# Kernel optimization log

Measured on AMD Instinct MI355X. Metric: run time of the kernel, lower is better.

## Reference

```python
import jax, jax.numpy as jnp
import numpy as np

N = 100000      # nodes
E = 1600000     # edges
IN = 128        # in_channels
H = 128         # hidden_channels
OUT = 40        # out_channels
EPS = 1e-5      # BatchNorm eps


def setup_inputs() -> dict:
    key = jax.random.key(0)
    ks = jax.random.split(key, 16)
    s_in = 1.0 / np.sqrt(IN)
    s_h = 1.0 / np.sqrt(H)
    s_fc = 1.0 / np.sqrt(IN + 2 * H)
    return {
        "x": jax.random.normal(ks[0], (N, IN), dtype=jnp.float32),
        "edge_index": jax.random.randint(ks[1], (2, E), 0, N, dtype=jnp.int32),
        "W1": jax.random.normal(ks[2], (IN, H), dtype=jnp.float32) * s_in,
        "b1": jnp.zeros((H,), dtype=jnp.float32),
        "W2": jax.random.normal(ks[3], (H, H), dtype=jnp.float32) * s_h,
        "b2": jnp.zeros((H,), dtype=jnp.float32),
        "bn1_gamma": jnp.ones((H,), dtype=jnp.float32),
        "bn1_beta": jnp.zeros((H,), dtype=jnp.float32),
        "bn1_mean": jax.random.normal(ks[4], (H,), dtype=jnp.float32) * 0.1,
        "bn1_var": jax.random.uniform(ks[5], (H,), dtype=jnp.float32, minval=0.5, maxval=1.5),
        "bn2_gamma": jnp.ones((H,), dtype=jnp.float32),
        "bn2_beta": jnp.zeros((H,), dtype=jnp.float32),
        "bn2_mean": jax.random.normal(ks[6], (H,), dtype=jnp.float32) * 0.1,
        "bn2_var": jax.random.uniform(ks[7], (H,), dtype=jnp.float32, minval=0.5, maxval=1.5),
        "fc_W": jax.random.normal(ks[8], (IN + 2 * H, OUT), dtype=jnp.float32) * s_fc,
        "fc_b": jnp.zeros((OUT,), dtype=jnp.float32),
    }


def _gcn_conv(x, edge_index, W, b):
    """PyG GCNConv: symmetric norm with self-loops. x:[N,F_in] -> [N,F_out]."""
    row, col = edge_index[0], edge_index[1]  # messages flow col -> row
    h = x @ W                                 # [N, F_out] transform first
    deg = jax.ops.segment_sum(jnp.ones((E,), x.dtype), row, num_segments=N) + 1.0  # +1 self-loop
    dinv = jax.lax.rsqrt(deg)                 # deg^{-1/2}
    norm = dinv[row] * dinv[col]              # [E]
    msg = h[col] * norm[:, None]              # gather + scale
    agg = jax.ops.segment_sum(msg, row, num_segments=N)
    agg = agg + h * (dinv * dinv)[:, None]    # self-loop contribution
    return agg + b


def _bn_eval(x, gamma, beta, mean, var):
    return (x - mean) * (gamma * jax.lax.rsqrt(var + EPS)) + beta


def reference(x, edge_index, W1, b1, W2, b2,
              bn1_gamma, bn1_beta, bn1_mean, bn1_var,
              bn2_gamma, bn2_beta, bn2_mean, bn2_var,
              fc_W, fc_b):
    x0 = x
    x1 = _gcn_conv(x0, edge_index, W1, b1)
    x1 = jax.nn.relu(_bn_eval(x1, bn1_gamma, bn1_beta, bn1_mean, bn1_var))
    # dropout: eval mode -> identity
    x2 = _gcn_conv(x1, edge_index, W2, b2)
    x2 = jax.nn.relu(_bn_eval(x2, bn2_gamma, bn2_beta, bn2_mean, bn2_var))
    out = jnp.concatenate([x0, x1, x2], axis=-1) @ fc_W + fc_b  # [N, OUT]
    return out
```

## Files before the change

kernel.cpp:

```cpp
#include <hip/hip_runtime.h>

#define N_NODES 100000
#define N_EDGES 1600000
#define C_H     128
#define C_OUT   40
#define K_FC    384
#define BN_EPS  1e-5f
#define NB      391
#define CHUNK   6144

typedef unsigned int uint;

__global__ void zero_i32(int* p, int n) {
    int i = blockIdx.x * blockDim.x + threadIdx.x;
    if (i < n) p[i] = 0;
}

__global__ __launch_bounds__(256) void bucket_count(const int* __restrict__ erow,
                                                    int* __restrict__ bcnt) {
    __shared__ int cnt[NB];
    for (int i = threadIdx.x; i < NB; i += 256) cnt[i] = 0;
    __syncthreads();
    const int c0 = blockIdx.x * CHUNK;
    const int c1 = min(c0 + CHUNK, N_EDGES);
    for (int e = c0 + threadIdx.x; e < c1; e += 256)
        atomicAdd(&cnt[erow[e] >> 8], 1);
    __syncthreads();
    for (int i = threadIdx.x; i < NB; i += 256)
        if (cnt[i]) atomicAdd(&bcnt[i], cnt[i]);
}

__global__ __launch_bounds__(256) void scan_buckets(const int* __restrict__ bcnt,
                                                    int* __restrict__ bstart,
                                                    int* __restrict__ bfill) {
    __shared__ int sa[512], sb[512];
    const int t = threadIdx.x;
    int v0 = (t < NB) ? bcnt[t] : 0;
    int v1 = (t + 256 < NB) ? bcnt[t + 256] : 0;
    sa[t] = v0; sa[t + 256] = v1;
    __syncthreads();
    int* src = sa; int* dst = sb;
    for (int off = 1; off < 512; off <<= 1) {
        dst[t]       = src[t]       + (t >= off ? src[t - off] : 0);
        dst[t + 256] = src[t + 256] + (t + 256 >= off ? src[t + 256 - off] : 0);
        __syncthreads();
        int* tmp = src; src = dst; dst = tmp;
    }
    if (t < NB)       { bstart[t] = src[t] - v0;             bfill[t] = src[t] - v0; }
    if (t + 256 < NB) { bstart[t + 256] = src[t + 256] - v1; bfill[t + 256] = src[t + 256] - v1; }
    if (t == 0) bstart[NB] = N_EDGES;
}

__global__ __launch_bounds__(256) void bucket_bin(const int* __restrict__ erow,
                                                  const int* __restrict__ ecol,
                                                  int* __restrict__ bfill,
                                                  int2* __restrict__ pairs) {
    __shared__ int cnt[NB];
    __shared__ int lpos[NB];
    for (int i = threadIdx.x; i < NB; i += 256) cnt[i] = 0;
    __syncthreads();
    const int c0 = blockIdx.x * CHUNK;
    const int c1 = min(c0 + CHUNK, N_EDGES);
    for (int e = c0 + threadIdx.x; e < c1; e += 256)
        atomicAdd(&cnt[erow[e] >> 8], 1);
    __syncthreads();
    for (int i = threadIdx.x; i < NB; i += 256)
        lpos[i] = cnt[i] ? atomicAdd(&bfill[i], cnt[i]) : 0;
    __syncthreads();
    for (int e = c0 + threadIdx.x; e < c1; e += 256) {
        int r = erow[e], c = ecol[e];
        int p = atomicAdd(&lpos[r >> 8], 1);
        pairs[p] = make_int2(r, c);
    }
}

__global__ __launch_bounds__(256) void bucket_csr(const int2* __restrict__ pairs,
                                                  const int* __restrict__ bstart,
                                                  int* __restrict__ rowptr,
                                                  float* __restrict__ dinv,
                                                  int* __restrict__ colsg) {
    __shared__ int lcnt[256], sa[256], sb[256], lpos[256];
    const int b = blockIdx.x;
    const int t = threadIdx.x;
    const int p0 = bstart[b], p1 = bstart[b + 1];
    lcnt[t] = 0;
    __syncthreads();
    for (int i = p0 + t; i < p1; i += 256)
        atomicAdd(&lcnt[pairs[i].x & 255], 1);
    __syncthreads();
    sa[t] = lcnt[t];
    __syncthreads();
    int* src = sa; int* dst = sb;
    for (int off = 1; off < 256; off <<= 1) {
        dst[t] = src[t] + (t >= off ? src[t - off] : 0);
        __syncthreads();
        int* tmp = src; src = dst; dst = tmp;
    }
    const int excl = src[t] - lcnt[t];
    const int r = b * 256 + t;
    if (r < N_NODES) {
        rowptr[r] = p0 + excl;
        dinv[r] = rsqrtf((float)lcnt[t] + 1.0f);
    }
    if (b == NB - 1 && t == 0) rowptr[N_NODES] = N_EDGES;
    lpos[t] = excl;
    __syncthreads();
    for (int i = p0 + t; i < p1; i += 256) {
        int2 pr = pairs[i];
        int s = atomicAdd(&lpos[pr.x & 255], 1);
        colsg[p0 + s] = pr.y;
    }
}

__global__ void bn_coef(const float* b1, const float* g1, const float* be1,
                        const float* m1, const float* v1,
                        const float* b2, const float* g2, const float* be2,
                        const float* m2, const float* v2,
                        float* s1, float* t1, float* s2, float* t2) {
    int f = threadIdx.x;
    float sa = g1[f] * rsqrtf(v1[f] + BN_EPS);
    s1[f] = sa;
    t1[f] = (b1[f] - m1[f]) * sa + be1[f];
    float sb = g2[f] * rsqrtf(v2[f] + BN_EPS);
    s2[f] = sb;
    t2[f] = (b2[f] - m2[f]) * sb + be2[f];
}

#define FMA4(A, S, V) \
    A.x = fmaf(S, V.x, A.x); A.y = fmaf(S, V.y, A.y); \
    A.z = fmaf(S, V.z, A.z); A.w = fmaf(S, V.w, A.w);

__device__ inline uint pack_bf16x2(float a, float b) {
    uint ua = __builtin_bit_cast(uint, a);
    uint ub = __builtin_bit_cast(uint, b);
    ua += 0x7fffu + ((ua >> 16) & 1u);
    ub += 0x7fffu + ((ub >> 16) & 1u);
    return (ua >> 16) | (ub & 0xffff0000u);
}

__global__ __launch_bounds__(256) void gemm_scaled(const float* __restrict__ X,
                                                   const float* __restrict__ W,
                                                   const float* __restrict__ dinv,
                                                   uint* __restrict__ Hs) {
    __shared__ float wl[64 * 128];
    __shared__ float xl[32 * 68];

    const int tid = threadIdx.x;
    const int rg = tid >> 5;
    const int c4 = (tid & 31) << 2;
    const int rb = blockIdx.x * 32;
    const int r0 = rb + rg * 4;

    float4 acc0 = {0,0,0,0}, acc1 = {0,0,0,0}, acc2 = {0,0,0,0}, acc3 = {0,0,0,0};

    for (int half = 0; half < 2; ++half) {
        const int k0 = half * 64;
        __syncthreads();
        {
            const float4* W4 = (const float4*)(W + (size_t)k0 * 128);
            float4* wl4 = (float4*)wl;
            #pragma unroll
            for (int i = 0; i < 8; ++i) wl4[tid + i * 256] = W4[tid + i * 256];
        }
        #pragma unroll
        for (int i = 0; i < 2; ++i) {
            int f = tid + i * 256;
            int row = f >> 4, cc = f & 15;
            float4 v = *(const float4*)(X + (size_t)(rb + row) * 128 + k0 + cc * 4);
            *(float4*)&xl[row * 68 + cc * 4] = v;
        }
        __syncthreads();

        for (int k4 = 0; k4 < 16; ++k4) {
            const float* wr = wl + k4 * 4 * 128 + c4;
            float4 w0 = *(const float4*)(wr);
            float4 w1 = *(const float4*)(wr + 128);
            float4 w2 = *(const float4*)(wr + 256);
            float4 w3 = *(const float4*)(wr + 384);
            float4 xv0 = *(const float4*)&xl[(rg * 4 + 0) * 68 + k4 * 4];
            float4 xv1 = *(const float4*)&xl[(rg * 4 + 1) * 68 + k4 * 4];
            float4 xv2 = *(const float4*)&xl[(rg * 4 + 2) * 68 + k4 * 4];
            float4 xv3 = *(const float4*)&xl[(rg * 4 + 3) * 68 + k4 * 4];
            FMA4(acc0, xv0.x, w0) FMA4(acc0, xv0.y, w1) FMA4(acc0, xv0.z, w2) FMA4(acc0, xv0.w, w3)
            FMA4(acc1, xv1.x, w0) FMA4(acc1, xv1.y, w1) FMA4(acc1, xv1.z, w2) FMA4(acc1, xv1.w, w3)
            FMA4(acc2, xv2.x, w0) FMA4(acc2, xv2.y, w1) FMA4(acc2, xv2.z, w2) FMA4(acc2, xv2.w, w3)
            FMA4(acc3, xv3.x, w0) FMA4(acc3, xv3.y, w1) FMA4(acc3, xv3.z, w2) FMA4(acc3, xv3.w, w3)
        }
    }
    float d0 = dinv[r0], d1 = dinv[r0 + 1], d2 = dinv[r0 + 2], d3 = dinv[r0 + 3];
    uint2 o;
    o.x = pack_bf16x2(acc0.x * d0, acc0.y * d0);
    o.y = pack_bf16x2(acc0.z * d0, acc0.w * d0);
    *(uint2*)(Hs + (size_t)(r0 + 0) * 64 + (c4 >> 1)) = o;
    o.x = pack_bf16x2(acc1.x * d1, acc1.y * d1);
    o.y = pack_bf16x2(acc1.z * d1, acc1.w * d1);
    *(uint2*)(Hs + (size_t)(r0 + 1) * 64 + (c4 >> 1)) = o;
    o.x = pack_bf16x2(acc2.x * d2, acc2.y * d2);
    o.y = pack_bf16x2(acc2.z * d2, acc2.w * d2);
    *(uint2*)(Hs + (size_t)(r0 + 2) * 64 + (c4 >> 1)) = o;
    o.x = pack_bf16x2(acc3.x * d3, acc3.y * d3);
    o.y = pack_bf16x2(acc3.z * d3, acc3.w * d3);
    *(uint2*)(Hs + (size_t)(r0 + 3) * 64 + (c4 >> 1)) = o;
}

#define ACC1(V) \
    accx += __builtin_bit_cast(float, V << 16); \
    accy += __builtin_bit_cast(float, V & 0xffff0000u);

__global__ __launch_bounds__(256) void spmm_bn_relu4(
    const uint* __restrict__ Hs, const int* __restrict__ cols,
    const int* __restrict__ rowptr, const float* __restrict__ dinv,
    const float* __restrict__ s, const float* __restrict__ t,
    float* __restrict__ Y) {
    const int lane = threadIdx.x & 63;
    const int r = blockIdx.x * 4 + (threadIdx.x >> 6);

    uint vself = Hs[(size_t)r * 64 + lane];
    float accx = __builtin_bit_cast(float, vself << 16);
    float accy = __builtin_bit_cast(float, vself & 0xffff0000u);
    const float di = dinv[r];
    const int e0 = rowptr[r], e1 = rowptr[r + 1];
    int j = e0;
    const int n16 = e0 + ((e1 - e0) & ~15);
    for (; j < n16; j += 16) {
        uint v[16];
        #pragma unroll
        for (int q = 0; q < 16; ++q)
            v[q] = Hs[(size_t)cols[j + q] * 64 + lane];
        #pragma unroll
        for (int q = 0; q < 16; ++q) { ACC1(v[q]) }
    }
    const int n4 = e0 + ((e1 - e0) & ~3);
    for (; j < n4; j += 4) {
        uint v[4];
        #pragma unroll
        for (int q = 0; q < 4; ++q)
            v[q] = Hs[(size_t)cols[j + q] * 64 + lane];
        #pragma unroll
        for (int q = 0; q < 4; ++q) { ACC1(v[q]) }
    }
    for (; j < e1; ++j) {
        uint v0 = Hs[(size_t)cols[j] * 64 + lane];
        ACC1(v0)
    }
    float2 sf = ((const float2*)s)[lane];
    float2 tf = ((const float2*)t)[lane];
    float2 o;
    o.x = fmaxf(fmaf(accx * di, sf.x, tf.x), 0.0f);
    o.y = fmaxf(fmaf(accy * di, sf.y, tf.y), 0.0f);
    ((float2*)Y)[(size_t)r * 64 + lane] = o;
}

__global__ __launch_bounds__(256) void final_gemm7(
    const float* __restrict__ X0, const float* __restrict__ X1,
    const float* __restrict__ X2, const float* __restrict__ fcW,
    const float* __restrict__ fcb, float* __restrict__ out) {
    __shared__ float xs[2][64 * 33];

    const int t = threadIdx.x;
    const int lane = t & 63;
    const int wq = __builtin_amdgcn_readfirstlane(t >> 6);
    const float* wbase = fcW + wq * 10;
    const int rbase = blockIdx.x * 64;

    float acc[10];
    #pragma unroll
    for (int c = 0; c < 10; ++c) acc[c] = 0.0f;

    const float* segs[3] = {X0, X1, X2};
    float4 xr[2];

    auto load_chunk = [&](int ch) {
        const float* xseg = segs[ch >> 2];
        const int koff = (ch & 3) * 32;
        #pragma unroll
        for (int i = 0; i < 2; ++i) {
            int f = t + i * 256;
            int row = f >> 3, cc = f & 7;
            int r = rbase + row;
            float4 v = {0, 0, 0, 0};
            if (r < N_NODES)
                v = *(const float4*)(xseg + (size_t)r * 128 + koff + cc * 4);
            xr[i] = v;
        }
    };

    auto store_chunk = [&](int buf) {
        #pragma unroll
        for (int i = 0; i < 2; ++i) {
            int f = t + i * 256;
            int row = f >> 3, cc = f & 7;
            float* p = &xs[buf][row * 33 + cc * 4];
            p[0] = xr[i].x; p[1] = xr[i].y; p[2] = xr[i].z; p[3] = xr[i].w;
        }
    };

    load_chunk(0);
    for (int ch = 0; ch < 12; ++ch) {
        const int buf = ch & 1;
        store_chunk(buf);
        if (ch < 11) load_chunk(ch + 1);
        __syncthreads();
        const int k0 = ch * 32;
        #pragma unroll
        for (int kk4 = 0; kk4 < 8; ++kk4) {
            float xv[4];
            #pragma unroll
            for (int j = 0; j < 4; ++j)
                xv[j] = xs[buf][lane * 33 + kk4 * 4 + j];
            #pragma unroll
            for (int j = 0; j < 4; ++j) {
                const float* wr = wbase + (size_t)(k0 + kk4 * 4 + j) * 40;
                #pragma unroll
                for (int c = 0; c < 10; ++c)
                    acc[c] = fmaf(xv[j], wr[c], acc[c]);
            }
        }
    }

    const int r = rbase + lane;
    if (r < N_NODES) {
        #pragma unroll
        for (int c2 = 0; c2 < 5; ++c2) {
            float2 o;
            o.x = acc[c2 * 2 + 0] + fcb[wq * 10 + c2 * 2 + 0];
            o.y = acc[c2 * 2 + 1] + fcb[wq * 10 + c2 * 2 + 1];
            *(float2*)(out + (size_t)r * 40 + wq * 10 + c2 * 2) = o;
        }
    }
}

extern "C" void kernel_launch(void* const* d_in, const int* in_sizes, int n_in,
                              void* d_out, int out_size, void* d_ws, size_t ws_size,
                              hipStream_t stream) {
    const float* x   = (const float*)d_in[0];
    const int*   ei  = (const int*)d_in[1];
    const int* e_row = ei;
    const int* e_col = ei + N_EDGES;
    const float* W1  = (const float*)d_in[2];
    const float* b1  = (const float*)d_in[3];
    const float* W2  = (const float*)d_in[4];
    const float* b2  = (const float*)d_in[5];
    const float* g1  = (const float*)d_in[6];
    const float* be1 = (const float*)d_in[7];
    const float* m1  = (const float*)d_in[8];
    const float* v1  = (const float*)d_in[9];
    const float* g2  = (const float*)d_in[10];
    const float* be2 = (const float*)d_in[11];
    const float* m2  = (const float*)d_in[12];
    const float* v2  = (const float*)d_in[13];
    const float* fcW = (const float*)d_in[14];
    const float* fcb = (const float*)d_in[15];
    float* out = (float*)d_out;

    char* ws = (char*)d_ws;
    size_t off = 0;
    auto alloc = [&](size_t b) {
        char* p = ws + off;
        off += (b + 255) & ~(size_t)255;
        return p;
    };
    uint*  h      = (uint*)alloc((size_t)N_NODES * C_H * 2);
    float* x1     = (float*)alloc((size_t)N_NODES * C_H * 4);
    float* x2     = (float*)alloc((size_t)N_NODES * C_H * 4);
    int2*  pairs  = (int2*)alloc((size_t)N_EDGES * 8);
    int*   cols   = (int*)alloc((size_t)N_EDGES * 4);
    float* dinv   = (float*)alloc(N_NODES * 4);
    int*   rowptr = (int*)alloc((N_NODES + 1) * 4);
    int*   bcnt   = (int*)alloc((NB + 1) * 4);
    int*   bstart = (int*)alloc((NB + 1) * 4);
    int*   bfill  = (int*)alloc((NB + 1) * 4);
    float* coef   = (float*)alloc(512 * 4);
    float* s1 = coef, *t1 = coef + 128, *s2 = coef + 256, *t2 = coef + 384;

    const int nwg_bin = (N_EDGES + CHUNK - 1) / CHUNK;

    zero_i32<<<2, 256, 0, stream>>>(bcnt, NB);
    bucket_count<<<nwg_bin, 256, 0, stream>>>(e_row, bcnt);
    scan_buckets<<<1, 256, 0, stream>>>(bcnt, bstart, bfill);
    bucket_bin<<<nwg_bin, 256, 0, stream>>>(e_row, e_col, bfill, pairs);
    bucket_csr<<<NB, 256, 0, stream>>>(pairs, bstart, rowptr, dinv, cols);
    bn_coef<<<1, 128, 0, stream>>>(b1, g1, be1, m1, v1, b2, g2, be2, m2, v2,
                                   s1, t1, s2, t2);

    gemm_scaled<<<N_NODES / 32, 256, 0, stream>>>(x, W1, dinv, h);
    spmm_bn_relu4<<<N_NODES / 4, 256, 0, stream>>>(h, cols, rowptr, dinv, s1, t1, x1);
    gemm_scaled<<<N_NODES / 32, 256, 0, stream>>>(x1, W2, dinv, h);
    spmm_bn_relu4<<<N_NODES / 4, 256, 0, stream>>>(h, cols, rowptr, dinv, s2, t2, x2);
    final_gemm7<<<(N_NODES + 63) / 64, 256, 0, stream>>>(x, x1, x2, fcW, fcb, out);
}
```

Baseline: 519.1 us.

## Triple-buffer final GEMM shared tiles with two-chunk-ahead register prefetch

```diff
diff --git a/kernel.cpp b/kernel.cpp
--- a/kernel.cpp
+++ b/kernel.cpp
@@ -251,11 +251,11 @@
     ((float2*)Y)[(size_t)r * 64 + lane] = o;
 }
 
-__global__ __launch_bounds__(256) void final_gemm7(
+__global__ __launch_bounds__(256) void final_gemm9(
     const float* __restrict__ X0, const float* __restrict__ X1,
     const float* __restrict__ X2, const float* __restrict__ fcW,
     const float* __restrict__ fcb, float* __restrict__ out) {
-    __shared__ float xs[2][64 * 33];
+    __shared__ float xs[3 * 64 * 33];
 
     const int t = threadIdx.x;
     const int lane = t & 63;
@@ -267,56 +267,78 @@
     #pragma unroll
     for (int c = 0; c < 10; ++c) acc[c] = 0.0f;
 
-    const float* segs[3] = {X0, X1, X2};
-    float4 xr[2];
-
-    auto load_chunk = [&](int ch) {
-        const float* xseg = segs[ch >> 2];
-        const int koff = (ch & 3) * 32;
-        #pragma unroll
-        for (int i = 0; i < 2; ++i) {
-            int f = t + i * 256;
-            int row = f >> 3, cc = f & 7;
-            int r = rbase + row;
-            float4 v = {0, 0, 0, 0};
-            if (r < N_NODES)
-                v = *(const float4*)(xseg + (size_t)r * 128 + koff + cc * 4);
-            xr[i] = v;
-        }
-    };
-
-    auto store_chunk = [&](int buf) {
-        #pragma unroll
-        for (int i = 0; i < 2; ++i) {
-            int f = t + i * 256;
-            int row = f >> 3, cc = f & 7;
-            float* p = &xs[buf][row * 33 + cc * 4];
-            p[0] = xr[i].x; p[1] = xr[i].y; p[2] = xr[i].z; p[3] = xr[i].w;
-        }
-    };
-
-    load_chunk(0);
-    for (int ch = 0; ch < 12; ++ch) {
-        const int buf = ch & 1;
-        store_chunk(buf);
-        if (ch < 11) load_chunk(ch + 1);
-        __syncthreads();
-        const int k0 = ch * 32;
-        #pragma unroll
-        for (int kk4 = 0; kk4 < 8; ++kk4) {
-            float xv[4];
-            #pragma unroll
-            for (int j = 0; j < 4; ++j)
-                xv[j] = xs[buf][lane * 33 + kk4 * 4 + j];
-            #pragma unroll
-            for (int j = 0; j < 4; ++j) {
-                const float* wr = wbase + (size_t)(k0 + kk4 * 4 + j) * 40;
-                #pragma unroll
-                for (int c = 0; c < 10; ++c)
-                    acc[c] = fmaf(xv[j], wr[c], acc[c]);
-            }
-        }
-    }
+    float4 A0, A1, B0, B1;
+
+#define LOADC(CH, R0, R1) do {                                               \
+    const float* xseg = ((CH) < 4) ? X0 : ((CH) < 8) ? X1 : X2;              \
+    const int koff_ = ((CH) & 3) * 32;                                       \
+    {   int f_ = t;       int row_ = f_ >> 3, cc_ = f_ & 7;                  \
+        int r_ = rbase + row_;                                               \
+        float4 v_ = {0, 0, 0, 0};                                            \
+        if (r_ < N_NODES)                                                    \
+            v_ = *(const float4*)(xseg + (size_t)r_ * 128 + koff_ + cc_ * 4);\
+        R0 = v_; }                                                           \
+    {   int f_ = t + 256; int row_ = f_ >> 3, cc_ = f_ & 7;                  \
+        int r_ = rbase + row_;                                               \
+        float4 v_ = {0, 0, 0, 0};                                            \
+        if (r_ < N_NODES)                                                    \
+            v_ = *(const float4*)(xseg + (size_t)r_ * 128 + koff_ + cc_ * 4);\
+        R1 = v_; }                                                           \
+} while (0)
+
+#define STOREC(SLOT, R0, R1) do {                                            \
+    float* base_ = xs + (SLOT) * 2112;                                       \
+    {   int f_ = t;       float* p_ = base_ + (f_ >> 3) * 33 + (f_ & 7) * 4; \
+        p_[0] = R0.x; p_[1] = R0.y; p_[2] = R0.z; p_[3] = R0.w; }            \
+    {   int f_ = t + 256; float* p_ = base_ + (f_ >> 3) * 33 + (f_ & 7) * 4; \
+        p_[0] = R1.x; p_[1] = R1.y; p_[2] = R1.z; p_[3] = R1.w; }            \
+} while (0)
+
+#define SYNC() do {                                                          \
+    asm volatile("s_waitcnt lgkmcnt(0)" ::: "memory");                       \
+    __builtin_amdgcn_sched_barrier(0);                                       \
+    __builtin_amdgcn_s_barrier();                                            \
+    __builtin_amdgcn_sched_barrier(0);                                       \
+} while (0)
+
+#define COMPUTEC(CH, SLOT) do {                                              \
+    const float* base_ = xs + (SLOT) * 2112 + lane * 33;                     \
+    const int k0_ = (CH) * 32;                                               \
+    _Pragma("unroll")                                                        \
+    for (int kk4 = 0; kk4 < 8; ++kk4) {                                      \
+        float xv_[4];                                                        \
+        _Pragma("unroll")                                                    \
+        for (int j = 0; j < 4; ++j) xv_[j] = base_[kk4 * 4 + j];             \
+        _Pragma("unroll")                                                    \
+        for (int j = 0; j < 4; ++j) {                                        \
+            const float* wr_ = wbase + (size_t)(k0_ + kk4 * 4 + j) * 40;     \
+            _Pragma("unroll")                                                \
+            for (int c = 0; c < 10; ++c)                                     \
+                acc[c] = fmaf(xv_[j], wr_[c], acc[c]);       \
+        }                                                                    \
+    }                                                                        \
+} while (0)
+
+    LOADC(0, A0, A1);
+    LOADC(1, B0, B1);
+    #pragma unroll
+    for (int p = 0; p < 6; ++p) {
+        const int ce = 2 * p, co = 2 * p + 1;
+        const int se = ce % 3, so = co % 3;
+        STOREC(se, A0, A1);
+        if (ce + 2 < 12) LOADC(ce + 2, A0, A1);
+        SYNC();
+        COMPUTEC(ce, se);
+        STOREC(so, B0, B1);
+        if (co + 2 < 12) LOADC(co + 2, B0, B1);
+        SYNC();
+        COMPUTEC(co, so);
+    }
+
+#undef LOADC
+#undef STOREC
+#undef SYNC
+#undef COMPUTEC
 
     const int r = rbase + lane;
     if (r < N_NODES) {
@@ -387,5 +409,5 @@
     spmm_bn_relu4<<<N_NODES / 4, 256, 0, stream>>>(h, cols, rowptr, dinv, s1, t1, x1);
     gemm_scaled<<<N_NODES / 32, 256, 0, stream>>>(x1, W2, dinv, h);
     spmm_bn_relu4<<<N_NODES / 4, 256, 0, stream>>>(h, cols, rowptr, dinv, s2, t2, x2);
-    final_gemm7<<<(N_NODES + 63) / 64, 256, 0, stream>>>(x, x1, x2, fcW, fcb, out);
-}
+    final_gemm9<<<(N_NODES + 63) / 64, 256, 0, stream>>>(x, x1, x2, fcW, fcb, out);
+}
```

New measurement: 878.1 us. 69.2% more time.
